# Kernel tuning notes

Hardware: AMD Instinct MI355X
Metric: run time of the kernel (lower is better)

Reference implementation:

```python
import jax, jax.numpy as jnp
import numpy as np
from jax import lax

FILTERS = [(1, 32), (2, 32), (3, 64), (4, 128), (5, 256), (6, 512), (7, 1024)]
CHAR_VOCAB, CHAR_DIM, MAX_CHARS = 262, 16, 50
N_FILTERS = sum(n for _, n in FILTERS)  # 2048
PROJ_DIM = 512
B, S = 16, 256


def setup_inputs() -> dict:
    key = jax.random.key(0)
    ks = jax.random.split(key, 32)
    inp = {}
    inp["words"] = jax.random.randint(ks[0], (B, S), 0, 50000)
    inp["chars"] = jax.random.randint(ks[1], (B, S, MAX_CHARS), 0, CHAR_VOCAB)
    inp["char_emb"] = jax.random.normal(ks[2], (CHAR_VOCAB, CHAR_DIM), jnp.float32) * 0.1
    for i, (w, n) in enumerate(FILTERS):
        inp[f"conv_w_{i}"] = jax.random.normal(ks[3 + i], (n, CHAR_DIM, w), jnp.float32) * 0.1
        inp[f"conv_b_{i}"] = jnp.zeros((n,), jnp.float32)
    for j in range(2):
        inp[f"hw_w_{j}"] = jax.random.normal(ks[12 + j], (2 * N_FILTERS, N_FILTERS), jnp.float32) * 0.02
        # Highway init: transform bias = 0, gate bias = 1
        inp[f"hw_b_{j}"] = jnp.concatenate([jnp.zeros((N_FILTERS,), jnp.float32), jnp.ones((N_FILTERS,), jnp.float32)])
    inp["proj_w"] = jax.random.normal(ks[20], (PROJ_DIM, N_FILTERS), jnp.float32) * 0.02
    inp["proj_b"] = jnp.zeros((PROJ_DIM,), jnp.float32)
    return inp


def _char_cnn(chars, char_emb, conv_ws, conv_bs, hw_ws, hw_bs, proj_w, proj_b):
    b, s, L = chars.shape
    # (B*S, CHAR_DIM, L)
    x = char_emb[chars].reshape(b * s, L, -1).transpose(0, 2, 1)
    convs = []
    for w, bias in zip(conv_ws, conv_bs):
        # Conv1d valid, NCW layout; y: (N, num, L-width+1)
        y = lax.conv_general_dilated(x, w, (1,), "VALID", dimension_numbers=("NCH", "OIH", "NCH"))
        y = y + bias[None, :, None]
        y = jnp.max(y, axis=-1)          # max over time
        convs.append(jax.nn.relu(y))      # activation
    h = jnp.concatenate(convs, axis=-1)   # (N, 2048)
    d = h.shape[-1]
    for W, bb in zip(hw_ws, hw_bs):
        p = h @ W.T + bb
        nonlinear = jax.nn.relu(p[:, :d])
        gate = jax.nn.sigmoid(p[:, d:])
        h = gate * h + (1.0 - gate) * nonlinear
    out = h @ proj_w.T + proj_b
    return out.reshape(b, s, -1)


def reference(words, chars, char_emb,
              conv_w_0, conv_b_0, conv_w_1, conv_b_1, conv_w_2, conv_b_2,
              conv_w_3, conv_b_3, conv_w_4, conv_b_4, conv_w_5, conv_b_5,
              conv_w_6, conv_b_6, hw_w_0, hw_b_0, hw_w_1, hw_b_1, proj_w, proj_b):
    conv_ws = [conv_w_0, conv_w_1, conv_w_2, conv_w_3, conv_w_4, conv_w_5, conv_w_6]
    conv_bs = [conv_b_0, conv_b_1, conv_b_2, conv_b_3, conv_b_4, conv_b_5, conv_b_6]
    return _char_cnn(chars, char_emb, conv_ws, conv_bs, [hw_w_0, hw_w_1], [hw_b_0, hw_b_1], proj_w, proj_b)
```

## Files before the change

kernel.cpp:

```cpp
#include <hip/hip_runtime.h>
#include <hip/hip_bf16.h>


#define NTOK 4096
#define NF   2048
#define KDIM 2048
#define HID  4096
#define PDIM 512

typedef __attribute__((ext_vector_type(4))) float floatx4;
typedef __attribute__((ext_vector_type(8))) short shortx8;

__device__ inline void async_copy16(const void* g, void* l) {
  __builtin_amdgcn_global_load_lds(
      (const __attribute__((address_space(1))) void*)(uintptr_t)g,
      (__attribute__((address_space(3))) void*)(uint32_t)(uintptr_t)l,
      16, 0, 0);
}

__global__ __launch_bounds__(256) void cvt_kernel(
    const float* __restrict__ s, __hip_bfloat16* __restrict__ d, int n) {
  int i = blockIdx.x * 256 + threadIdx.x;
  if (i < n) d[i] = __float2bfloat16(s[i]);
}

__global__ __launch_bounds__(256) void cvt_hw(
    const float* __restrict__ s, __hip_bfloat16* __restrict__ d) {
  int i = blockIdx.x * 256 + threadIdx.x;
  int r = i >> 11, k = i & 2047;
  int sr = (r >> 1) + (r & 1) * 2048;
  d[i] = __float2bfloat16(s[(size_t)sr * 2048 + k]);
}

__global__ __launch_bounds__(256) void conv_wprep(
    const float* __restrict__ w0, const float* __restrict__ w1,
    const float* __restrict__ w2, const float* __restrict__ w3,
    const float* __restrict__ w4, const float* __restrict__ w5,
    const float* __restrict__ w6,
    const float* __restrict__ b0, const float* __restrict__ b1,
    const float* __restrict__ b2, const float* __restrict__ b3,
    const float* __restrict__ b4, const float* __restrict__ b5,
    const float* __restrict__ b6, const float* __restrict__ emb,
    __hip_bfloat16* __restrict__ Wb, float* __restrict__ Bc,
    __hip_bfloat16* __restrict__ embb) {
  int idx = blockIdx.x * 256 + threadIdx.x;
  const int start[7] = {0, 32, 64, 128, 256, 512, 1024};
  const float* ws[7] = {w0, w1, w2, w3, w4, w5, w6};
  const float* bs[7] = {b0, b1, b2, b3, b4, b5, b6};
  if (idx < 262144) {
    int ch = idx >> 7, kp = idx & 127;
    int f = (ch >= 32) + (ch >= 64) + (ch >= 128) + (ch >= 256) +
            (ch >= 512) + (ch >= 1024);
    int w = f + 1, lc = ch - start[f];
    int d = kp & 15, k = kp >> 4;
    float v = (k < w) ? ws[f][((size_t)lc * 16 + d) * w + k] : 0.f;
    Wb[idx] = __float2bfloat16(v);
  } else if (idx < 262144 + 2048) {
    int ch = idx - 262144;
    int f = (ch >= 32) + (ch >= 64) + (ch >= 128) + (ch >= 256) +
            (ch >= 512) + (ch >= 1024);
    Bc[ch] = bs[f][ch - start[f]];
  } else if (idx < 262144 + 2048 + 4192) {
    int e = idx - 262144 - 2048;
    embb[e] = __float2bfloat16(emb[e]);
  }
}

template <int NKT, int NT>
__device__ __forceinline__ void conv_body(
    const __hip_bfloat16* __restrict__ embb,
    const __hip_bfloat16* __restrict__ Wb, const float* __restrict__ bias,
    __hip_bfloat16* __restrict__ h, int chb,
    __hip_bfloat16 (*Xs)[4][72 * 24], int* cidx) {
  int tid = threadIdx.x, wave = tid >> 6, lane = tid & 63;
  int frow = lane & 15, q = lane >> 4;
  int tokbase = blockIdx.x * 32;

  shortx8 wreg[NKT][4];
#pragma unroll
  for (int kt = 0; kt < NKT; ++kt)
#pragma unroll
    for (int j = 0; j < 4; ++j)
      wreg[kt][j] = *(const shortx8*)(
          Wb + (size_t)(chb + j * 16 + frow) * 128 + kt * 32 + q * 8);

  float blane = bias[chb + lane];
  int Tvj[4];
#pragma unroll
  for (int j = 0; j < 4; ++j) {
    int ch = chb + j * 16 + frow;
    int w = 1 + (ch >= 32) + (ch >= 64) + (ch >= 128) + (ch >= 256) +
            (ch >= 512) + (ch >= 1024);
    Tvj[j] = 51 - w;
  }

  auto stage = [&](int g, int buf) {
#pragma unroll
    for (int rep = 0; rep < 2; ++rep) {
      int rr = tid + rep * 256;
      if (rr < 288) {
        int tk = rr / 72, r = rr - tk * 72;
        if (r < 50) {
          int c = cidx[(g * 4 + tk) * 50 + r];
          const shortx8* e = (const shortx8*)(embb + c * 16);
          *(shortx8*)(&Xs[buf][tk][r * 24]) = e[0];
          *(shortx8*)(&Xs[buf][tk][r * 24 + 8]) = e[1];
        } else if (g <= 1) {
          shortx8 z = {0, 0, 0, 0, 0, 0, 0, 0};
          *(shortx8*)(&Xs[buf][tk][r * 24]) = z;
          *(shortx8*)(&Xs[buf][tk][r * 24 + 8]) = z;
        }
      }
    }
  };

  stage(0, 0);
  __syncthreads();

  const floatx4 zero = {0.f, 0.f, 0.f, 0.f};
#pragma unroll 1
  for (int g = 0; g < 8; ++g) {
    if (g < 7) stage(g + 1, (g + 1) & 1);

    const __hip_bfloat16* Xw = &Xs[g & 1][wave][0];
    floatx4 acc[NT][4];

#pragma unroll
    for (int kt = 0; kt < NKT; ++kt) {
      int kk = kt * 2 + (q >> 1);
      int d0 = (q & 1) * 8;
      shortx8 xf[NT];
#pragma unroll
      for (int i = 0; i < NT; ++i)
        xf[i] = *(const shortx8*)(Xw + (i * 16 + frow + kk) * 24 + d0);
#pragma unroll
      for (int i = 0; i < NT; ++i)
#pragma unroll
        for (int j = 0; j < 4; ++j) {
          if (kt == 0)
            acc[i][j] = __builtin_amdgcn_mfma_f32_16x16x32_bf16(
                xf[i], wreg[0][j], zero, 0, 0, 0);
          else
            acc[i][j] = __builtin_amdgcn_mfma_f32_16x16x32_bf16(
                xf[i], wreg[kt][j], acc[i][j], 0, 0, 0);
        }
    }

    float vj[4];
#pragma unroll
    for (int j = 0; j < 4; ++j) {
      float v = -1e30f;
#pragma unroll
      for (int i = 0; i < NT; ++i) {
#pragma unroll
        for (int r = 0; r < 4; ++r) {
          if (i < 2) {
            v = fmaxf(v, acc[i][j][r]);
          } else {
            int t = i * 16 + q * 4 + r;
            if (t < Tvj[j]) v = fmaxf(v, acc[i][j][r]);
          }
        }
      }
      v = fmaxf(v, __shfl_xor(v, 16));
      v = fmaxf(v, __shfl_xor(v, 32));
      vj[j] = v;
    }
    float r0 = (q & 2) ? vj[2] : vj[0];
    float r1 = (q & 2) ? vj[3] : vj[1];
    float rv = (q & 1) ? r1 : r0;
    int tok = tokbase + g * 4 + wave;
    h[(size_t)tok * NF + chb + lane] =
        __float2bfloat16(fmaxf(rv + blane, 0.f));
    __syncthreads();
  }
}

__global__ __launch_bounds__(256) void conv_all(
    const int* __restrict__ chars, const __hip_bfloat16* __restrict__ embb,
    const __hip_bfloat16* __restrict__ Wb, const float* __restrict__ bias,
    __hip_bfloat16* __restrict__ h) {
  __shared__ __align__(16) __hip_bfloat16 Xs[2][4][72 * 24];
  __shared__ __align__(16) int cidx[32 * 50];
  int tid = threadIdx.x;
  for (int c = tid; c < 400; c += 256) {
    int4 v = *(const int4*)(chars + (size_t)blockIdx.x * 1600 + c * 4);
    *(int4*)(cidx + c * 4) = v;
  }
  __syncthreads();

  int by = blockIdx.y;
  if (by == 0)
    conv_body<1, 4>(embb, Wb, bias, h, 0, Xs, cidx);
  else if (by < 4)
    conv_body<2, 3>(embb, Wb, bias, h, 64 + (by - 1) * 64, Xs, cidx);
  else if (by < 16)
    conv_body<3, 3>(embb, Wb, bias, h, 256 + (by - 4) * 64, Xs, cidx);
  else
    conv_body<4, 3>(embb, Wb, bias, h, 1024 + (by - 16) * 64, Xs, cidx);
}

__global__ __launch_bounds__(256) void gemm_hw(
    const __hip_bfloat16* __restrict__ A, const __hip_bfloat16* __restrict__ B,
    const float* __restrict__ hwb, __hip_bfloat16* __restrict__ Hdst) {
  const int K = KDIM;
  __shared__ __align__(16) __hip_bfloat16 As[128 * 32];
  __shared__ __align__(16) __hip_bfloat16 Bs[128 * 32];
  int tid = threadIdx.x;
  int wave = tid >> 6, lane = tid & 63;
  int wr = wave >> 1, wc = wave & 1;
  int bn = blockIdx.y, bm = blockIdx.x;

  int srow = lane >> 2;
  int skq  = (lane & 3) * 8;
  int frow = lane & 15;
  int fkq  = (lane >> 4) * 8;

  floatx4 acc[4][4];
  floatx4 zero = {0.f, 0.f, 0.f, 0.f};
#pragma unroll
  for (int i = 0; i < 4; ++i)
#pragma unroll
    for (int j = 0; j < 4; ++j) acc[i][j] = zero;

  const __hip_bfloat16* Ab = A + (size_t)bn * 128 * K;
  const __hip_bfloat16* Bb = B + (size_t)bm * 128 * K;

  for (int kb = 0; kb < K; kb += 32) {
    __syncthreads();
#pragma unroll
    for (int it = 0; it < 2; ++it) {
      int seg = wave * 2 + it;
      async_copy16(Ab + (size_t)(seg * 16 + srow) * K + kb + skq,
                   (char*)As + seg * 1024);
      async_copy16(Bb + (size_t)(seg * 16 + srow) * K + kb + skq,
                   (char*)Bs + seg * 1024);
    }
    __syncthreads();

    shortx8 af[4], bf[4];
#pragma unroll
    for (int i = 0; i < 4; ++i)
      af[i] = *(const shortx8*)(As + (wr * 64 + i * 16 + frow) * 32 + fkq);
#pragma unroll
    for (int j = 0; j < 4; ++j)
      bf[j] = *(const shortx8*)(Bs + (wc * 64 + j * 16 + frow) * 32 + fkq);
#pragma unroll
    for (int i = 0; i < 4; ++i)
#pragma unroll
      for (int j = 0; j < 4; ++j)
        acc[i][j] =
            __builtin_amdgcn_mfma_f32_16x16x32_bf16(af[i], bf[j], acc[i][j], 0, 0, 0);
  }

  int crow0 = bn * 128 + wr * 64 + (lane >> 4) * 4;
  int ccol0 = bm * 128 + wc * 64 + (lane & 15);
#pragma unroll
  for (int i = 0; i < 4; ++i)
#pragma unroll
    for (int j = 0; j < 4; ++j) {
      int gcol = ccol0 + j * 16;
      float bb = (gcol & 1) ? hwb[2048 + (gcol >> 1)] : hwb[gcol >> 1];
#pragma unroll
      for (int r = 0; r < 4; ++r) {
        int row = crow0 + i * 16 + r;
        float v = acc[i][j][r] + bb;
        float partner = __shfl_xor(v, 1);
        if (!(lane & 1)) {
          float gte = 1.f / (1.f + expf(-partner));
          int ch = gcol >> 1;
          float hold = __bfloat162float(A[(size_t)row * 2048 + ch]);
          float hnew = gte * hold + (1.f - gte) * fmaxf(v, 0.f);
          Hdst[(size_t)row * 2048 + ch] = __float2bfloat16(hnew);
        }
      }
    }
}

__global__ __launch_bounds__(256) void gemm_proj(
    const __hip_bfloat16* __restrict__ A, const __hip_bfloat16* __restrict__ B,
    float* __restrict__ C, const float* __restrict__ bias, int M) {
  const int K = KDIM;
  __shared__ __align__(16) __hip_bfloat16 As[128 * 32];
  __shared__ __align__(16) __hip_bfloat16 Bs[128 * 32];
  int tid = threadIdx.x;
  int wave = tid >> 6, lane = tid & 63;
  int wr = wave >> 1, wc = wave & 1;
  int bn = blockIdx.y, bm = blockIdx.x;

  int srow = lane >> 2;
  int skq  = (lane & 3) * 8;
  int frow = lane & 15;
  int fkq  = (lane >> 4) * 8;

  floatx4 acc[4][4];
  floatx4 zero = {0.f, 0.f, 0.f, 0.f};
#pragma unroll
  for (int i = 0; i < 4; ++i)
#pragma unroll
    for (int j = 0; j < 4; ++j) acc[i][j] = zero;

  const __hip_bfloat16* Ab = A + (size_t)bn * 128 * K;
  const __hip_bfloat16* Bb = B + (size_t)bm * 128 * K;

  for (int kb = 0; kb < K; kb += 32) {
    __syncthreads();
#pragma unroll
    for (int it = 0; it < 2; ++it) {
      int seg = wave * 2 + it;
      async_copy16(Ab + (size_t)(seg * 16 + srow) * K + kb + skq,
                   (char*)As + seg * 1024);
      async_copy16(Bb + (size_t)(seg * 16 + srow) * K + kb + skq,
                   (char*)Bs + seg * 1024);
    }
    __syncthreads();

    shortx8 af[4], bf[4];
#pragma unroll
    for (int i = 0; i < 4; ++i)
      af[i] = *(const shortx8*)(As + (wr * 64 + i * 16 + frow) * 32 + fkq);
#pragma unroll
    for (int j = 0; j < 4; ++j)
      bf[j] = *(const shortx8*)(Bs + (wc * 64 + j * 16 + frow) * 32 + fkq);
#pragma unroll
    for (int i = 0; i < 4; ++i)
#pragma unroll
      for (int j = 0; j < 4; ++j)
        acc[i][j] =
            __builtin_amdgcn_mfma_f32_16x16x32_bf16(af[i], bf[j], acc[i][j], 0, 0, 0);
  }

  int crow0 = bn * 128 + wr * 64 + (lane >> 4) * 4;
  int ccol0 = bm * 128 + wc * 64 + (lane & 15);
#pragma unroll
  for (int i = 0; i < 4; ++i)
#pragma unroll
    for (int j = 0; j < 4; ++j) {
      int c = ccol0 + j * 16;
#pragma unroll
      for (int r = 0; r < 4; ++r) {
        int row = crow0 + i * 16 + r;
        C[(size_t)row * M + c] = acc[i][j][r] + bias[c];
      }
    }
}

extern "C" void kernel_launch(void* const* d_in, const int* in_sizes, int n_in,
                              void* d_out, int out_size, void* d_ws, size_t ws_size,
                              hipStream_t stream) {
  const int*   chars  = (const int*)d_in[1];
  const float* emb    = (const float*)d_in[2];
  const float* cw[7];
  const float* cb[7];
  for (int i = 0; i < 7; ++i) {
    cw[i] = (const float*)d_in[3 + 2 * i];
    cb[i] = (const float*)d_in[4 + 2 * i];
  }
  const float* hw_w0  = (const float*)d_in[17];
  const float* hw_b0  = (const float*)d_in[18];
  const float* hw_w1  = (const float*)d_in[19];
  const float* hw_b1  = (const float*)d_in[20];
  const float* proj_w = (const float*)d_in[21];
  const float* proj_b = (const float*)d_in[22];
  float* out = (float*)d_out;

  char* ws = (char*)d_ws;
  __hip_bfloat16* h      = (__hip_bfloat16*)(ws);
  __hip_bfloat16* h2     = (__hip_bfloat16*)(ws + (16ull << 20));
  __hip_bfloat16* convWb = (__hip_bfloat16*)(ws + (32ull << 20));
  float*          convBc = (float*)(ws + (32ull << 20) + 524288);
  __hip_bfloat16* embb   = (__hip_bfloat16*)(ws + (32ull << 20) + 524288 + 8192);
  __hip_bfloat16* w0b    = (__hip_bfloat16*)(ws + (48ull << 20));
  __hip_bfloat16* w1b    = (__hip_bfloat16*)(ws + (64ull << 20));
  __hip_bfloat16* pwb    = (__hip_bfloat16*)(ws + (80ull << 20));

  cvt_hw<<<(HID * KDIM) / 256, 256, 0, stream>>>(hw_w0, w0b);
  cvt_hw<<<(HID * KDIM) / 256, 256, 0, stream>>>(hw_w1, w1b);
  cvt_kernel<<<(PDIM * KDIM) / 256, 256, 0, stream>>>(proj_w, pwb, PDIM * KDIM);
  conv_wprep<<<(262144 + 2048 + 4192 + 255) / 256, 256, 0, stream>>>(
      cw[0], cw[1], cw[2], cw[3], cw[4], cw[5], cw[6],
      cb[0], cb[1], cb[2], cb[3], cb[4], cb[5], cb[6], emb,
      convWb, convBc, embb);

  conv_all<<<dim3(NTOK / 32, 32), 256, 0, stream>>>(chars, embb, convWb,
                                                    convBc, h);

  gemm_hw<<<dim3(HID / 128, NTOK / 128), 256, 0, stream>>>(h, w0b, hw_b0, h2);
  gemm_hw<<<dim3(HID / 128, NTOK / 128), 256, 0, stream>>>(h2, w1b, hw_b1, h);
  gemm_proj<<<dim3(PDIM / 128, NTOK / 128), 256, 0, stream>>>(h, pwb, out,
                                                              proj_b, PDIM);
}
```

Baseline: 536.5 us.

## Split conv into per-width kernels, widen GEMM K-tile with XOR swizzle, shrink proj tiles

The fused conv kernel is split into four templated launches so each width group gets its own smaller LDS footprint (56 staged rows instead of 72 where possible), and char indices are read directly from global memory. The highway GEMMs now stage 64-wide K tiles with an XOR-swizzled LDS layout, which halves the number of barriers and is meant to avoid LDS bank conflicts. The projection GEMM uses 32-row M tiles so more blocks run on the small 512-wide output. The trade-offs are extra kernel launches and uncached chars reads.

```diff
diff --git a/kernel.cpp b/kernel.cpp
--- a/kernel.cpp
+++ b/kernel.cpp
@@ -66,14 +66,15 @@
   }
 }
 
-template <int NKT, int NT>
-__device__ __forceinline__ void conv_body(
-    const __hip_bfloat16* __restrict__ embb,
+template <int NKT, int NT, int ROWS>
+__global__ __launch_bounds__(256) void conv_k(
+    const int* __restrict__ chars, const __hip_bfloat16* __restrict__ embb,
     const __hip_bfloat16* __restrict__ Wb, const float* __restrict__ bias,
-    __hip_bfloat16* __restrict__ h, int chb,
-    __hip_bfloat16 (*Xs)[4][72 * 24], int* cidx) {
+    __hip_bfloat16* __restrict__ h, int chbase) {
+  __shared__ __align__(16) __hip_bfloat16 Xs[2 * 4 * ROWS * 24];
   int tid = threadIdx.x, wave = tid >> 6, lane = tid & 63;
   int frow = lane & 15, q = lane >> 4;
+  int chb = chbase + blockIdx.y * 64;
   int tokbase = blockIdx.x * 32;
 
   shortx8 wreg[NKT][4];
@@ -95,20 +96,22 @@
   }
 
   auto stage = [&](int g, int buf) {
-#pragma unroll
-    for (int rep = 0; rep < 2; ++rep) {
+    constexpr int NST = 4 * ROWS;
+#pragma unroll
+    for (int rep = 0; rep < (NST + 255) / 256; ++rep) {
       int rr = tid + rep * 256;
-      if (rr < 288) {
-        int tk = rr / 72, r = rr - tk * 72;
+      if (rr < NST) {
+        int tk = rr / ROWS, r = rr - tk * ROWS;
+        __hip_bfloat16* dst = Xs + ((size_t)(buf * 4 + tk) * ROWS + r) * 24;
         if (r < 50) {
-          int c = cidx[(g * 4 + tk) * 50 + r];
+          int c = chars[(size_t)(tokbase + g * 4 + tk) * 50 + r];
           const shortx8* e = (const shortx8*)(embb + c * 16);
-          *(shortx8*)(&Xs[buf][tk][r * 24]) = e[0];
-          *(shortx8*)(&Xs[buf][tk][r * 24 + 8]) = e[1];
+          *(shortx8*)(dst) = e[0];
+          *(shortx8*)(dst + 8) = e[1];
         } else if (g <= 1) {
           shortx8 z = {0, 0, 0, 0, 0, 0, 0, 0};
-          *(shortx8*)(&Xs[buf][tk][r * 24]) = z;
-          *(shortx8*)(&Xs[buf][tk][r * 24 + 8]) = z;
+          *(shortx8*)(dst) = z;
+          *(shortx8*)(dst + 8) = z;
         }
       }
     }
@@ -122,7 +125,7 @@
   for (int g = 0; g < 8; ++g) {
     if (g < 7) stage(g + 1, (g + 1) & 1);
 
-    const __hip_bfloat16* Xw = &Xs[g & 1][wave][0];
+    const __hip_bfloat16* Xw = Xs + (size_t)((g & 1) * 4 + wave) * ROWS * 24;
     floatx4 acc[NT][4];
 
 #pragma unroll
@@ -176,45 +179,21 @@
   }
 }
 
-__global__ __launch_bounds__(256) void conv_all(
-    const int* __restrict__ chars, const __hip_bfloat16* __restrict__ embb,
-    const __hip_bfloat16* __restrict__ Wb, const float* __restrict__ bias,
-    __hip_bfloat16* __restrict__ h) {
-  __shared__ __align__(16) __hip_bfloat16 Xs[2][4][72 * 24];
-  __shared__ __align__(16) int cidx[32 * 50];
-  int tid = threadIdx.x;
-  for (int c = tid; c < 400; c += 256) {
-    int4 v = *(const int4*)(chars + (size_t)blockIdx.x * 1600 + c * 4);
-    *(int4*)(cidx + c * 4) = v;
-  }
-  __syncthreads();
-
-  int by = blockIdx.y;
-  if (by == 0)
-    conv_body<1, 4>(embb, Wb, bias, h, 0, Xs, cidx);
-  else if (by < 4)
-    conv_body<2, 3>(embb, Wb, bias, h, 64 + (by - 1) * 64, Xs, cidx);
-  else if (by < 16)
-    conv_body<3, 3>(embb, Wb, bias, h, 256 + (by - 4) * 64, Xs, cidx);
-  else
-    conv_body<4, 3>(embb, Wb, bias, h, 1024 + (by - 16) * 64, Xs, cidx);
-}
-
 __global__ __launch_bounds__(256) void gemm_hw(
     const __hip_bfloat16* __restrict__ A, const __hip_bfloat16* __restrict__ B,
     const float* __restrict__ hwb, __hip_bfloat16* __restrict__ Hdst) {
   const int K = KDIM;
-  __shared__ __align__(16) __hip_bfloat16 As[128 * 32];
-  __shared__ __align__(16) __hip_bfloat16 Bs[128 * 32];
+  __shared__ __align__(16) __hip_bfloat16 As[128 * 64];
+  __shared__ __align__(16) __hip_bfloat16 Bs[128 * 64];
   int tid = threadIdx.x;
   int wave = tid >> 6, lane = tid & 63;
   int wr = wave >> 1, wc = wave & 1;
   int bn = blockIdx.y, bm = blockIdx.x;
 
-  int srow = lane >> 2;
-  int skq  = (lane & 3) * 8;
+  int sr8 = lane >> 3;
+  int sc8 = lane & 7;
   int frow = lane & 15;
-  int fkq  = (lane >> 4) * 8;
+  int q    = lane >> 4;
 
   floatx4 acc[4][4];
   floatx4 zero = {0.f, 0.f, 0.f, 0.f};
@@ -226,35 +205,42 @@
   const __hip_bfloat16* Ab = A + (size_t)bn * 128 * K;
   const __hip_bfloat16* Bb = B + (size_t)bm * 128 * K;
 
-  for (int kb = 0; kb < K; kb += 32) {
-    __syncthreads();
-#pragma unroll
-    for (int it = 0; it < 2; ++it) {
-      int seg = wave * 2 + it;
-      async_copy16(Ab + (size_t)(seg * 16 + srow) * K + kb + skq,
-                   (char*)As + seg * 1024);
-      async_copy16(Bb + (size_t)(seg * 16 + srow) * K + kb + skq,
-                   (char*)Bs + seg * 1024);
-    }
-    __syncthreads();
-
-    shortx8 af[4], bf[4];
-#pragma unroll
-    for (int i = 0; i < 4; ++i)
-      af[i] = *(const shortx8*)(As + (wr * 64 + i * 16 + frow) * 32 + fkq);
-#pragma unroll
-    for (int j = 0; j < 4; ++j)
-      bf[j] = *(const shortx8*)(Bs + (wc * 64 + j * 16 + frow) * 32 + fkq);
-#pragma unroll
-    for (int i = 0; i < 4; ++i)
-#pragma unroll
-      for (int j = 0; j < 4; ++j)
-        acc[i][j] =
-            __builtin_amdgcn_mfma_f32_16x16x32_bf16(af[i], bf[j], acc[i][j], 0, 0, 0);
-  }
-
-  int crow0 = bn * 128 + wr * 64 + (lane >> 4) * 4;
-  int ccol0 = bm * 128 + wc * 64 + (lane & 15);
+  for (int kb = 0; kb < K; kb += 64) {
+    __syncthreads();
+#pragma unroll
+    for (int it = 0; it < 4; ++it) {
+      int seg = wave * 4 + it;
+      int r = seg * 8 + sr8;
+      int gc = sc8 ^ (r & 7);
+      async_copy16(Ab + (size_t)r * K + kb + gc * 8, (char*)As + seg * 1024);
+      async_copy16(Bb + (size_t)r * K + kb + gc * 8, (char*)Bs + seg * 1024);
+    }
+    __syncthreads();
+
+#pragma unroll
+    for (int s = 0; s < 2; ++s) {
+      shortx8 af[4], bf[4];
+#pragma unroll
+      for (int i = 0; i < 4; ++i) {
+        int r = wr * 64 + i * 16 + frow;
+        af[i] = *(const shortx8*)(As + r * 64 + ((s * 4 + q) ^ (r & 7)) * 8);
+      }
+#pragma unroll
+      for (int j = 0; j < 4; ++j) {
+        int r = wc * 64 + j * 16 + frow;
+        bf[j] = *(const shortx8*)(Bs + r * 64 + ((s * 4 + q) ^ (r & 7)) * 8);
+      }
+#pragma unroll
+      for (int i = 0; i < 4; ++i)
+#pragma unroll
+        for (int j = 0; j < 4; ++j)
+          acc[i][j] = __builtin_amdgcn_mfma_f32_16x16x32_bf16(
+              af[i], bf[j], acc[i][j], 0, 0, 0);
+    }
+  }
+
+  int crow0 = bn * 128 + wr * 64 + q * 4;
+  int ccol0 = bm * 128 + wc * 64 + frow;
 #pragma unroll
   for (int i = 0; i < 4; ++i)
 #pragma unroll
@@ -279,70 +265,72 @@
 
 __global__ __launch_bounds__(256) void gemm_proj(
     const __hip_bfloat16* __restrict__ A, const __hip_bfloat16* __restrict__ B,
-    float* __restrict__ C, const float* __restrict__ bias, int M) {
+    float* __restrict__ C, const float* __restrict__ bias) {
   const int K = KDIM;
-  __shared__ __align__(16) __hip_bfloat16 As[128 * 32];
-  __shared__ __align__(16) __hip_bfloat16 Bs[128 * 32];
+  __shared__ __align__(16) __hip_bfloat16 As[32 * 64];
+  __shared__ __align__(16) __hip_bfloat16 Bs[128 * 64];
   int tid = threadIdx.x;
   int wave = tid >> 6, lane = tid & 63;
   int wr = wave >> 1, wc = wave & 1;
   int bn = blockIdx.y, bm = blockIdx.x;
 
-  int srow = lane >> 2;
-  int skq  = (lane & 3) * 8;
-  int frow = lane & 15;
-  int fkq  = (lane >> 4) * 8;
-
-  floatx4 acc[4][4];
+  int sr8 = lane >> 3, sc8 = lane & 7;
+  int frow = lane & 15, q = lane >> 4;
+
+  floatx4 acc[4];
   floatx4 zero = {0.f, 0.f, 0.f, 0.f};
 #pragma unroll
-  for (int i = 0; i < 4; ++i)
-#pragma unroll
-    for (int j = 0; j < 4; ++j) acc[i][j] = zero;
-
-  const __hip_bfloat16* Ab = A + (size_t)bn * 128 * K;
+  for (int j = 0; j < 4; ++j) acc[j] = zero;
+
+  const __hip_bfloat16* Ab = A + (size_t)bn * 32 * K;
   const __hip_bfloat16* Bb = B + (size_t)bm * 128 * K;
 
-  for (int kb = 0; kb < K; kb += 32) {
-    __syncthreads();
-#pragma unroll
-    for (int it = 0; it < 2; ++it) {
-      int seg = wave * 2 + it;
-      async_copy16(Ab + (size_t)(seg * 16 + srow) * K + kb + skq,
-                   (char*)As + seg * 1024);
-      async_copy16(Bb + (size_t)(seg * 16 + srow) * K + kb + skq,
-                   (char*)Bs + seg * 1024);
-    }
-    __syncthreads();
-
-    shortx8 af[4], bf[4];
-#pragma unroll
-    for (int i = 0; i < 4; ++i)
-      af[i] = *(const shortx8*)(As + (wr * 64 + i * 16 + frow) * 32 + fkq);
-#pragma unroll
-    for (int j = 0; j < 4; ++j)
-      bf[j] = *(const shortx8*)(Bs + (wc * 64 + j * 16 + frow) * 32 + fkq);
-#pragma unroll
-    for (int i = 0; i < 4; ++i)
+  for (int kb = 0; kb < K; kb += 64) {
+    __syncthreads();
+    {
+      int r = wave * 8 + sr8;
+      int gc = sc8 ^ (r & 7);
+      async_copy16(Ab + (size_t)r * K + kb + gc * 8, (char*)As + wave * 1024);
+    }
+#pragma unroll
+    for (int it = 0; it < 4; ++it) {
+      int seg = wave * 4 + it;
+      int r = seg * 8 + sr8;
+      int gc = sc8 ^ (r & 7);
+      async_copy16(Bb + (size_t)r * K + kb + gc * 8, (char*)Bs + seg * 1024);
+    }
+    __syncthreads();
+
+#pragma unroll
+    for (int s = 0; s < 2; ++s) {
+      shortx8 af, bf[4];
+      {
+        int r = wr * 16 + frow;
+        af = *(const shortx8*)(As + r * 64 + ((s * 4 + q) ^ (r & 7)) * 8);
+      }
+#pragma unroll
+      for (int j = 0; j < 4; ++j) {
+        int r = wc * 64 + j * 16 + frow;
+        bf[j] = *(const shortx8*)(Bs + r * 64 + ((s * 4 + q) ^ (r & 7)) * 8);
+      }
 #pragma unroll
       for (int j = 0; j < 4; ++j)
-        acc[i][j] =
-            __builtin_amdgcn_mfma_f32_16x16x32_bf16(af[i], bf[j], acc[i][j], 0, 0, 0);
-  }
-
-  int crow0 = bn * 128 + wr * 64 + (lane >> 4) * 4;
-  int ccol0 = bm * 128 + wc * 64 + (lane & 15);
-#pragma unroll
-  for (int i = 0; i < 4; ++i)
-#pragma unroll
-    for (int j = 0; j < 4; ++j) {
-      int c = ccol0 + j * 16;
-#pragma unroll
-      for (int r = 0; r < 4; ++r) {
-        int row = crow0 + i * 16 + r;
-        C[(size_t)row * M + c] = acc[i][j][r] + bias[c];
-      }
-    }
+        acc[j] = __builtin_amdgcn_mfma_f32_16x16x32_bf16(af, bf[j], acc[j],
+                                                          0, 0, 0);
+    }
+  }
+
+  int crow0 = bn * 32 + wr * 16 + q * 4;
+  int ccol0 = bm * 128 + wc * 64 + frow;
+#pragma unroll
+  for (int j = 0; j < 4; ++j) {
+    int c = ccol0 + j * 16;
+#pragma unroll
+    for (int r = 0; r < 4; ++r) {
+      int row = crow0 + r;
+      C[(size_t)row * PDIM + c] = acc[j][r] + bias[c];
+    }
+  }
 }
 
 extern "C" void kernel_launch(void* const* d_in, const int* in_sizes, int n_in,
@@ -382,11 +370,17 @@
       cb[0], cb[1], cb[2], cb[3], cb[4], cb[5], cb[6], emb,
       convWb, convBc, embb);
 
-  conv_all<<<dim3(NTOK / 32, 32), 256, 0, stream>>>(chars, embb, convWb,
-                                                    convBc, h);
+  conv_k<1, 4, 72><<<dim3(128, 1), 256, 0, stream>>>(chars, embb, convWb,
+                                                     convBc, h, 0);
+  conv_k<2, 3, 56><<<dim3(128, 3), 256, 0, stream>>>(chars, embb, convWb,
+                                                     convBc, h, 64);
+  conv_k<3, 3, 56><<<dim3(128, 12), 256, 0, stream>>>(chars, embb, convWb,
+                                                      convBc, h, 256);
+  conv_k<4, 3, 56><<<dim3(128, 16), 256, 0, stream>>>(chars, embb, convWb,
+                                                      convBc, h, 1024);
 
   gemm_hw<<<dim3(HID / 128, NTOK / 128), 256, 0, stream>>>(h, w0b, hw_b0, h2);
   gemm_hw<<<dim3(HID / 128, NTOK / 128), 256, 0, stream>>>(h2, w1b, hw_b1, h);
-  gemm_proj<<<dim3(PDIM / 128, NTOK / 128), 256, 0, stream>>>(h, pwb, out,
-                                                              proj_b, PDIM);
-}
+  gemm_proj<<<dim3(PDIM / 128, NTOK / 32), 256, 0, stream>>>(h, pwb, out,
+                                                             proj_b);
+}
```

After: 520.4 us. 1.03x faster.
